# Kernel optimization log

Measured on AMD Instinct MI355X. Metric: run time of the kernel, lower is better.

The kernel has to match this reference:

```python
import jax, jax.numpy as jnp
import numpy as np

B, H, S, D = 1, 16, 4096, 64


def setup_inputs() -> dict:
    key = jax.random.key(0)
    kq, kk, kv = jax.random.split(key, 3)
    Q = jax.random.normal(kq, (B, H, S, D), dtype=jnp.float32)
    K = jax.random.normal(kk, (B, H, S, D), dtype=jnp.float32)
    V = jax.random.normal(kv, (B, H, S, D), dtype=jnp.float32)
    # causal mask, broadcast over batch/heads: True = attend
    mask = jnp.tril(jnp.ones((S, S), dtype=bool))[None, None, :, :]
    return {"Q": Q, "K": K, "V": V, "mask": mask}


def reference(Q, K, V, mask):
    d_k = Q.shape[-1]
    scale = 1.0 / jnp.sqrt(jnp.asarray(d_k, dtype=Q.dtype))
    # [..., q, k] scores; mask==False positions set to -inf before softmax
    scores = jnp.einsum('...qd,...kd->...qk', Q, K) * scale
    scores = jnp.where(mask, scores, jnp.asarray(-jnp.inf, dtype=scores.dtype))
    attn = jax.nn.softmax(scores, axis=-1)
    return jnp.einsum('...qk,...kd->...qd', attn, V)
```

## Files before the change

kernel.cpp:

```cpp
#include <hip/hip_runtime.h>
#include <hip/hip_bf16.h>

typedef __attribute__((ext_vector_type(8))) short short8;
typedef __attribute__((ext_vector_type(4))) short s4v;
typedef __attribute__((ext_vector_type(4))) int   int4v;
typedef __attribute__((ext_vector_type(4))) float floatx4;

#define MFMA16(A,B,C) __builtin_amdgcn_mfma_f32_16x16x32_bf16(A,B,C,0,0,0)

__device__ __forceinline__ short bf16bits(float x) {
    __hip_bfloat16 h = __float2bfloat16(x);
    return *(short*)&h;
}
__device__ __forceinline__ short8 cvt8(const float* p) {
    floatx4 a = *(const floatx4*)p;
    floatx4 b = *(const floatx4*)(p + 4);
    short8 r;
    r[0]=bf16bits(a.x); r[1]=bf16bits(a.y); r[2]=bf16bits(a.z); r[3]=bf16bits(a.w);
    r[4]=bf16bits(b.x); r[5]=bf16bits(b.y); r[6]=bf16bits(b.z); r[7]=bf16bits(b.w);
    return r;
}
__device__ __forceinline__ short8 cvt8s(const float* p) {
    constexpr float SCL2 = 0.125f * 1.44269504088896f;
    floatx4 a = *(const floatx4*)p;
    floatx4 b = *(const floatx4*)(p + 4);
    a *= SCL2; b *= SCL2;
    short8 r;
    r[0]=bf16bits(a.x); r[1]=bf16bits(a.y); r[2]=bf16bits(a.z); r[3]=bf16bits(a.w);
    r[4]=bf16bits(b.x); r[5]=bf16bits(b.y); r[6]=bf16bits(b.z); r[7]=bf16bits(b.w);
    return r;
}
__device__ __forceinline__ int pk2(float lo, float hi) {
    int r;
    asm("v_cvt_pk_bf16_f32 %0, %1, %2" : "=v"(r) : "v"(lo), "v"(hi));
    return r;
}

__global__ __launch_bounds__(256) void prep(const float* __restrict__ V,
                                            short* __restrict__ VT,
                                            const float* __restrict__ K,
                                            short* __restrict__ K16, int doK)
{
    __shared__ short tile[64 * 65];
    const int t  = threadIdx.x;
    const int h  = blockIdx.x >> 6;
    const int s0 = (blockIdx.x & 63) << 6;
    const float* src = V + ((size_t)h * 4096 + s0) * 64;
    const int r = t >> 4, dq = (t & 15) * 4;
#pragma unroll
    for (int pass = 0; pass < 4; ++pass) {
        const int s = pass * 16 + r;
        floatx4 f = *(const floatx4*)(src + s * 64 + dq);
        short* w = tile + s * 65 + dq;
        w[0] = bf16bits(f.x); w[1] = bf16bits(f.y);
        w[2] = bf16bits(f.z); w[3] = bf16bits(f.w);
    }
    __syncthreads();
    const int d = t >> 2, sc = (t & 3) * 16;
    short8 a, b;
#pragma unroll
    for (int j = 0; j < 8; ++j) a[j] = tile[(sc + j) * 65 + d];
#pragma unroll
    for (int j = 0; j < 8; ++j) b[j] = tile[(sc + 8 + j) * 65 + d];
    short* dst = VT + ((size_t)h * 64 + d) * 4096 + s0 + sc;
    *(short8*)dst       = a;
    *(short8*)(dst + 8) = b;
    if (doK) {
        const size_t base = (size_t)blockIdx.x * 4096 + (size_t)t * 16;
        *(short8*)(K16 + base)     = cvt8(K + base);
        *(short8*)(K16 + base + 8) = cvt8(K + base + 8);
    }
}

template<bool KB16>
__global__ __attribute__((amdgpu_waves_per_eu(4, 4))) __launch_bounds__(256)
void attn_fast(const float* __restrict__ Qg, const float* __restrict__ Kg,
               const short* __restrict__ K16g, const short* __restrict__ VTg,
               float* __restrict__ Og)
{
    constexpr int S = 4096, D = 64;

    __shared__ __align__(16) short lK[4096];
    __shared__ __align__(16) short lV[4096];
    __shared__ __align__(16) float lM[5120];

    const int tid = threadIdx.x;
    const int wv  = tid >> 6;
    const int ln  = tid & 63;
    const int ll  = ln & 15;
    const int qd  = ln >> 4;
    const int qhalf = wv & 1;
    const int khalf = wv >> 1;

    const int c = blockIdx.x & 255;
    const int s = blockIdx.x >> 8;
    const int h = c & 15;
    const int x = c >> 4;
    const int qblk = (s == 0) ? (63 - x) : (s == 1) ? (32 + x) : (s == 2) ? (31 - x) : x;
    const int qb   = qblk << 6;
    const int qrow = qb + (qhalf << 5);

    const float* Qh  = Qg  + (size_t)h * S * D;
    const float* Kf  = Kg  + (size_t)h * S * D;
    const short* K16 = K16g + (size_t)h * S * D;
    const short* Vt  = VTg + (size_t)h * 64 * S;

    short8 qA0, qA1, qB0, qB1;
    {
        const float* qp = Qh + (qrow + ll) * D + qd * 8;
        qA0 = cvt8s(qp);       qA1 = cvt8s(qp + 32);
        const float* qp2 = qp + 16 * D;
        qB0 = cvt8s(qp2);      qB1 = cvt8s(qp2 + 32);
    }

    floatx4 oA[4], oB[4], olA, olB;
#pragma unroll
    for (int dt = 0; dt < 4; ++dt) { oA[dt] = (floatx4){0.f,0.f,0.f,0.f}; oB[dt] = oA[dt]; }
    olA = (floatx4){0.f,0.f,0.f,0.f};
    olB = olA;

    short8 ones;
#pragma unroll
    for (int j = 0; j < 8; ++j) ones[j] = (short)0x3F80;

    const int kkey = tid >> 3, kd8 = tid & 7;
    const int koct = kd8 & 3;
    short* kdst = lK + ((kkey >> 4) * 2 + (kd8 >> 2)) * 512
                     + ((((kkey & 15) | (koct << 4)) ^ (koct * 5)) * 8);
    const float* ksrcf = Kf  + kkey * 64 + kd8 * 8;
    const short* ksrc6 = K16 + kkey * 64 + kd8 * 8;
    const int vd = tid >> 2, voct = tid & 3;
    short* vdst = lV + (vd >> 4) * 512
                     + ((((vd & 15) | (voct << 4)) ^ (voct * 5)) * 8);
    const short* vsrc = Vt + (size_t)vd * S + voct * 8;
    const int rblk = ((ll | (qd << 4)) ^ (qd * 5));

    const int kv_end = qb + 64;
    const int wv_end = qrow + 32;

    auto ldK = [&](int kv) -> short8 {
        return KB16 ? *(const short8*)(ksrc6 + kv * 64) : cvt8(ksrcf + kv * 64);
    };

    auto mkpf = [&](floatx4 sc0, floatx4 sc1, int qgrp, int kvh) -> short8 {
        float p0[4], p1[4];
#pragma unroll
        for (int r = 0; r < 4; ++r) { p0[r] = exp2f(sc0[r]); p1[r] = exp2f(sc1[r]); }
        if (kvh + 31 > qgrp) {
            const int qg = qgrp + ll;
            const int k0 = kvh + qd * 4, k1 = k0 + 16;
#pragma unroll
            for (int r = 0; r < 4; ++r) {
                if (k0 + r > qg) p0[r] = 0.f;
                if (k1 + r > qg) p1[r] = 0.f;
            }
        }
        int w0 = pk2(p0[0], p0[1]);
        int w1 = pk2(p0[2], p0[3]);
        int w2 = pk2(p1[0], p1[1]);
        int w3 = pk2(p1[2], p1[3]);
        asm("v_permlane32_swap_b32 %0, %1" : "+v"(w0), "+v"(w2));
        asm("v_permlane32_swap_b32 %0, %1" : "+v"(w1), "+v"(w3));
        asm("v_permlane16_swap_b32 %0, %1" : "+v"(w0), "+v"(w2));
        asm("v_permlane16_swap_b32 %0, %1" : "+v"(w1), "+v"(w3));
        int4v pv = {w0, w1, w2, w3};
        return *(short8*)&pv;
    };

    short8 kpre0 = ldK(0),  kpre1 = ldK(32);
    short8 vpre0 = *(const short8*)(vsrc);
    short8 vpre1 = *(const short8*)(vsrc + 32);

    for (int kv = 0; kv < kv_end; kv += 64) {
        __syncthreads();
        *(short8*)kdst          = kpre0;
        *(short8*)(kdst + 2048) = kpre1;
        *(short8*)vdst          = vpre0;
        *(short8*)(vdst + 2048) = vpre1;
        __syncthreads();
        if (kv + 64 < kv_end) {
            kpre0 = ldK(kv + 64);
            kpre1 = ldK(kv + 96);
            vpre0 = *(const short8*)(vsrc + kv + 64);
            vpre1 = *(const short8*)(vsrc + kv + 96);
        }

        const int kvw = kv + (khalf << 5);
        if (kvw < wv_end) {
            const short* Kb = lK + (khalf << 11);
            const short* Vb = lV + (khalf << 11);
            floatx4 zz = (floatx4){0.f,0.f,0.f,0.f};
            floatx4 sA0=zz, sA1=zz, sB0=zz, sB1=zz;
            short8 kf;
            __builtin_amdgcn_s_setprio(1);
            kf = ((const short8*)(Kb +    0))[rblk]; sA0 = MFMA16(kf, qA0, sA0); sB0 = MFMA16(kf, qB0, sB0);
            kf = ((const short8*)(Kb +  512))[rblk]; sA0 = MFMA16(kf, qA1, sA0); sB0 = MFMA16(kf, qB1, sB0);
            kf = ((const short8*)(Kb + 1024))[rblk]; sA1 = MFMA16(kf, qA0, sA1); sB1 = MFMA16(kf, qB0, sB1);
            kf = ((const short8*)(Kb + 1536))[rblk]; sA1 = MFMA16(kf, qA1, sA1); sB1 = MFMA16(kf, qB1, sB1);
            __builtin_amdgcn_s_setprio(0);

            short8 pfA = mkpf(sA0, sA1, qrow,      kvw);
            short8 pfB = mkpf(sB0, sB1, qrow + 16, kvw);
            __builtin_amdgcn_s_setprio(1);
#pragma unroll
            for (int dt = 0; dt < 4; ++dt) {
                short8 vf = ((const short8*)(Vb + dt * 512))[rblk];
                oA[dt] = MFMA16(pfA, vf, oA[dt]);
                oB[dt] = MFMA16(pfB, vf, oB[dt]);
            }
            olA = MFMA16(pfA, ones, olA);
            olB = MFMA16(pfB, ones, olB);
            __builtin_amdgcn_s_setprio(0);
        }
    }

    __syncthreads();
    const int mbase = ((qhalf << 6) + ln) * 40;
    if (khalf == 1) {
#pragma unroll
        for (int dt = 0; dt < 4; ++dt)
#pragma unroll
            for (int r = 0; r < 4; ++r) {
                lM[mbase + dt * 4 + r]      = oA[dt][r];
                lM[mbase + 20 + dt * 4 + r] = oB[dt][r];
            }
#pragma unroll
        for (int r = 0; r < 4; ++r) {
            lM[mbase + 16 + r] = olA[r];
            lM[mbase + 36 + r] = olB[r];
        }
    }
    __syncthreads();
    if (khalf == 0) {
#pragma unroll
        for (int dt = 0; dt < 4; ++dt)
#pragma unroll
            for (int r = 0; r < 4; ++r) {
                oA[dt][r] += lM[mbase + dt * 4 + r];
                oB[dt][r] += lM[mbase + 20 + dt * 4 + r];
            }
#pragma unroll
        for (int r = 0; r < 4; ++r) {
            olA[r] += lM[mbase + 16 + r];
            olB[r] += lM[mbase + 36 + r];
        }
#pragma unroll
        for (int r = 0; r < 4; ++r) {
            const float rl = 1.f / fmaxf(olA[r], 1e-37f);
            const int q = qrow + qd * 4 + r;
            float* op = Og + ((size_t)h * S + q) * D + ll;
#pragma unroll
            for (int dt = 0; dt < 4; ++dt)
                op[dt * 16] = oA[dt][r] * rl;
        }
#pragma unroll
        for (int r = 0; r < 4; ++r) {
            const float rl = 1.f / fmaxf(olB[r], 1e-37f);
            const int q = qrow + 16 + qd * 4 + r;
            float* op = Og + ((size_t)h * S + q) * D + ll;
#pragma unroll
            for (int dt = 0; dt < 4; ++dt)
                op[dt * 16] = oB[dt][r] * rl;
        }
    }
}

__global__ __launch_bounds__(256, 4)
void attn_legacy(const float* __restrict__ Qg, const float* __restrict__ Kg,
                 const float* __restrict__ Vg, float* __restrict__ Og)
{
    constexpr int S = 4096, D = 64;
    constexpr float SCL2 = 0.125f * 1.44269504088896f;
    constexpr float NEG  = -1.0e30f;
    __shared__ __align__(16) short lK[2048];
    __shared__ __align__(16) short lV[2048];
    __shared__ __align__(16) short lP[2048];
    const int tid = threadIdx.x, wv = tid >> 6, ln = tid & 63, ll = ln & 15, qd = ln >> 4;
    const int bid = blockIdx.x, h = bid & 15, qblk = 63 - (bid >> 4), qb = qblk << 6;
    const float* Qh = Qg + (size_t)h * S * D;
    const float* Kh = Kg + (size_t)h * S * D;
    const float* Vh = Vg + (size_t)h * S * D;
    const int qrow = qb + wv * 16;
    short8 qf0, qf1;
    { const float* qp = Qh + (qrow + ll) * D + qd * 8; qf0 = cvt8(qp); qf1 = cvt8(qp + 32); }
    floatx4 o[4]; float mi[4], li[4];
#pragma unroll
    for (int dt = 0; dt < 4; ++dt) o[dt] = (floatx4){0.f,0.f,0.f,0.f};
#pragma unroll
    for (int r = 0; r < 4; ++r) { mi[r] = NEG; li[r] = 0.f; }
    const int k_st = tid >> 3, dbase = (tid & 7) * 8;
    const int sq = (dbase >> 3) & 3, sks = dbase >> 5;
    const int kw_slot = (((k_st >> 4) * 2 + sks) * 64)
                      + (((sq << 4) | (k_st & 15)) ^ (sq | (sks << 2)));
    const int kr0 = ln ^ qd, kr1 = ln ^ (qd | 4), vbit3 = (ln >> 3) & 1;
    const int kv_end = qb + 64, wv_end = qrow + 16;
    for (int kv = 0; kv < kv_end; kv += 32) {
        __syncthreads();
        {
            short8 kval = cvt8(Kh + (kv + k_st) * D + dbase);
            ((short8*)lK)[kw_slot] = kval;
            short8 vval = cvt8(Vh + (kv + k_st) * D + dbase);
            const int vq = (k_st >> 3) << 4, vj = k_st & 7;
#pragma unroll
            for (int i = 0; i < 8; ++i) {
                int d = dbase + i, dt = d >> 4, l2 = d & 15;
                int lp = (vq | l2) ^ (((l2 >> 3) & 1) | (dt << 1));
                lV[dt * 512 + lp * 8 + vj] = vval[i];
            }
        }
        __syncthreads();
        if (kv < wv_end) {
            floatx4 sc0 = (floatx4){0.f,0.f,0.f,0.f}, sc1 = sc0; short8 kf;
            kf = ((const short8*)lK)[0*64+kr0]; sc0 = MFMA16(qf0, kf, sc0);
            kf = ((const short8*)lK)[1*64+kr1]; sc0 = MFMA16(qf1, kf, sc0);
            kf = ((const short8*)lK)[2*64+kr0]; sc1 = MFMA16(qf0, kf, sc1);
            kf = ((const short8*)lK)[3*64+kr1]; sc1 = MFMA16(qf1, kf, sc1);
            float p0[4], p1[4]; const int qg = qrow + qd * 4;
#pragma unroll
            for (int r = 0; r < 4; ++r) { p0[r] = sc0[r]*SCL2; p1[r] = sc1[r]*SCL2; }
            if (kv + 31 > qrow) {
                const int k0 = kv + ll, k1 = kv + 16 + ll;
#pragma unroll
                for (int r = 0; r < 4; ++r) {
                    if (k0 > qg + r) p0[r] = NEG;
                    if (k1 > qg + r) p1[r] = NEG;
                }
            }
#pragma unroll
            for (int r = 0; r < 4; ++r) {
                float mx = fmaxf(p0[r], p1[r]);
                mx = fmaxf(mx, __shfl_xor(mx,1)); mx = fmaxf(mx, __shfl_xor(mx,2));
                mx = fmaxf(mx, __shfl_xor(mx,4)); mx = fmaxf(mx, __shfl_xor(mx,8));
                const float nm = fmaxf(mi[r], mx);
                const float a = exp2f(mi[r] - nm); mi[r] = nm;
                p0[r] = exp2f(p0[r] - nm); p1[r] = exp2f(p1[r] - nm);
                float ps = p0[r] + p1[r];
                ps += __shfl_xor(ps,1); ps += __shfl_xor(ps,2);
                ps += __shfl_xor(ps,4); ps += __shfl_xor(ps,8);
                li[r] = li[r] * a + ps;
#pragma unroll
                for (int dt = 0; dt < 4; ++dt) o[dt][r] *= a;
            }
            {
                const int pbase = wv * 512 + (ll & 7);
                const int dl0 = ((ll >> 3) << 4) + qd * 4;
#pragma unroll
                for (int r = 0; r < 4; ++r) {
                    lP[pbase + (dl0 + r) * 8]      = bf16bits(p0[r]);
                    lP[pbase + (dl0 + 32 + r) * 8] = bf16bits(p1[r]);
                }
            }
            __threadfence_block();
            short8 pf = ((const short8*)lP)[wv * 64 + ln];
#pragma unroll
            for (int dt = 0; dt < 4; ++dt) {
                short8 vf = ((const short8*)lV)[dt * 64 + (ln ^ (vbit3 | (dt << 1)))];
                o[dt] = MFMA16(pf, vf, o[dt]);
            }
        }
    }
#pragma unroll
    for (int r = 0; r < 4; ++r) {
        const float rl = 1.f / fmaxf(li[r], 1e-30f);
        const int q = qrow + qd * 4 + r;
        float* op = Og + ((size_t)h * S + q) * D + ll;
#pragma unroll
        for (int dt = 0; dt < 4; ++dt) op[dt * 16] = o[dt][r] * rl;
    }
}

extern "C" void kernel_launch(void* const* d_in, const int* in_sizes, int n_in,
                              void* d_out, int out_size, void* d_ws, size_t ws_size,
                              hipStream_t stream) {
    const float* Q = (const float*)d_in[0];
    const float* K = (const float*)d_in[1];
    const float* V = (const float*)d_in[2];
    float* O = (float*)d_out;
    const size_t elems  = (size_t)16 * 4096 * 64;
    const size_t oneBuf = elems * sizeof(short);
    if (ws_size >= 2 * oneBuf) {
        short* VT  = (short*)d_ws;
        short* K16 = (short*)d_ws + elems;
        prep<<<dim3(1024), dim3(256), 0, stream>>>(V, VT, K, K16, 1);
        attn_fast<true><<<dim3(1024), dim3(256), 0, stream>>>(Q, K, K16, VT, O);
    } else if (ws_size >= oneBuf) {
        short* VT = (short*)d_ws;
        prep<<<dim3(1024), dim3(256), 0, stream>>>(V, VT, K, VT, 0);
        attn_fast<false><<<dim3(1024), dim3(256), 0, stream>>>(Q, K, nullptr, VT, O);
    } else {
        attn_legacy<<<dim3(1024), dim3(256), 0, stream>>>(Q, K, V, O);
    }
}
```

Measured before the change: 185.2 us.

## Double-buffer K/V tiles in LDS using direct global-to-LDS loads

Replaces register-staged K/V prefetch with global_load_lds direct transfers into a double-buffered LDS ring, which removes one of the two barriers per iteration and the register round-trip. The source addresses are remapped so the direct-load layout keeps the swizzled pattern. The end-of-kernel reduction scratch now reuses the K/V buffers, and waves_per_eu is raised from 4 to 5. The risks are the larger LDS footprint, the tighter register budget, and correctness of the one-barrier scheme, since the next-buffer writes are ordered only by the single barrier at the top of the loop.

```diff
diff --git a/kernel.cpp b/kernel.cpp
--- a/kernel.cpp
+++ b/kernel.cpp
@@ -34,6 +34,11 @@
     int r;
     asm("v_cvt_pk_bf16_f32 %0, %1, %2" : "=v"(r) : "v"(lo), "v"(hi));
     return r;
+}
+__device__ __forceinline__ void g2l16(const short* g, short* l) {
+    __builtin_amdgcn_global_load_lds(
+        (const __attribute__((address_space(1))) void*)g,
+        (__attribute__((address_space(3))) void*)l, 16, 0, 0);
 }
 
 __global__ __launch_bounds__(256) void prep(const float* __restrict__ V,
@@ -73,16 +78,15 @@
 }
 
 template<bool KB16>
-__global__ __attribute__((amdgpu_waves_per_eu(4, 4))) __launch_bounds__(256)
+__global__ __attribute__((amdgpu_waves_per_eu(5, 5))) __launch_bounds__(256)
 void attn_fast(const float* __restrict__ Qg, const float* __restrict__ Kg,
                const short* __restrict__ K16g, const short* __restrict__ VTg,
                float* __restrict__ Og)
 {
     constexpr int S = 4096, D = 64;
 
-    __shared__ __align__(16) short lK[4096];
-    __shared__ __align__(16) short lV[4096];
-    __shared__ __align__(16) float lM[5120];
+    __shared__ __align__(16) short lK[8192];
+    __shared__ __align__(16) short lV[8192];
 
     const int tid = threadIdx.x;
     const int wv  = tid >> 6;
@@ -123,24 +127,29 @@
 #pragma unroll
     for (int j = 0; j < 8; ++j) ones[j] = (short)0x3F80;
 
-    const int kkey = tid >> 3, kd8 = tid & 7;
-    const int koct = kd8 & 3;
-    short* kdst = lK + ((kkey >> 4) * 2 + (kd8 >> 2)) * 512
-                     + ((((kkey & 15) | (koct << 4)) ^ (koct * 5)) * 8);
-    const float* ksrcf = Kf  + kkey * 64 + kd8 * 8;
-    const short* ksrc6 = K16 + kkey * 64 + kd8 * 8;
-    const int vd = tid >> 2, voct = tid & 3;
-    short* vdst = lV + (vd >> 4) * 512
-                     + ((((vd & 15) | (voct << 4)) ^ (voct * 5)) * 8);
-    const short* vsrc = Vt + (size_t)vd * S + voct * 8;
+    int kOff0, kOff1, vOff0, vOff1;
+    const float *kFp0, *kFp1;
+#define DECODE_SLOT(J, KOF, VOF, KFP) {                                        \
+        const int slot = (wv * 2 + (J)) * 64 + ln;                             \
+        const int hh = slot >> 8, bb = (slot >> 6) & 3, sw = slot & 63;        \
+        const int ko = (sw >> 4) & 3;                                          \
+        const int kkey = hh * 32 + (bb >> 1) * 16 + ((sw ^ (ko * 5)) & 15);    \
+        const int kd8  = ((bb & 1) << 2) | ko;                                 \
+        const int vd   = bb * 16 + ((sw ^ (ko * 5)) & 15);                     \
+        KOF = kkey * 64 + kd8 * 8;                                             \
+        VOF = vd * S + hh * 32 + ko * 8;                                       \
+        KFP = Kf + (size_t)kkey * D + kd8 * 8;                                 \
+    }
+    DECODE_SLOT(0, kOff0, vOff0, kFp0)
+    DECODE_SLOT(1, kOff1, vOff1, kFp1)
+#undef DECODE_SLOT
+    const int dstA = (wv * 2 + 0) * 512;
+    const int dstB = (wv * 2 + 1) * 512;
+
     const int rblk = ((ll | (qd << 4)) ^ (qd * 5));
 
     const int kv_end = qb + 64;
     const int wv_end = qrow + 32;
-
-    auto ldK = [&](int kv) -> short8 {
-        return KB16 ? *(const short8*)(ksrc6 + kv * 64) : cvt8(ksrcf + kv * 64);
-    };
 
     auto mkpf = [&](floatx4 sc0, floatx4 sc1, int qgrp, int kvh) -> short8 {
         float p0[4], p1[4];
@@ -167,28 +176,47 @@
         return *(short8*)&pv;
     };
 
-    short8 kpre0 = ldK(0),  kpre1 = ldK(32);
-    short8 vpre0 = *(const short8*)(vsrc);
-    short8 vpre1 = *(const short8*)(vsrc + 32);
-
+    short8 kApre, kBpre;
+    g2l16(Vt + vOff0, lV + dstA);
+    g2l16(Vt + vOff1, lV + dstB);
+    if constexpr (KB16) {
+        g2l16(K16 + kOff0, lK + dstA);
+        g2l16(K16 + kOff1, lK + dstB);
+    } else {
+        *(short8*)(lK + dstA + ln * 8) = cvt8(kFp0);
+        *(short8*)(lK + dstB + ln * 8) = cvt8(kFp1);
+        if (64 < kv_end) {
+            kApre = cvt8(kFp0 + (size_t)64 * D);
+            kBpre = cvt8(kFp1 + (size_t)64 * D);
+        }
+    }
+
+    int bo = 0;
     for (int kv = 0; kv < kv_end; kv += 64) {
         __syncthreads();
-        *(short8*)kdst          = kpre0;
-        *(short8*)(kdst + 2048) = kpre1;
-        *(short8*)vdst          = vpre0;
-        *(short8*)(vdst + 2048) = vpre1;
-        __syncthreads();
+        const int nbo = bo ^ 4096;
         if (kv + 64 < kv_end) {
-            kpre0 = ldK(kv + 64);
-            kpre1 = ldK(kv + 96);
-            vpre0 = *(const short8*)(vsrc + kv + 64);
-            vpre1 = *(const short8*)(vsrc + kv + 96);
+            const short* Vs = Vt + (kv + 64);
+            g2l16(Vs + vOff0, lV + nbo + dstA);
+            g2l16(Vs + vOff1, lV + nbo + dstB);
+            if constexpr (KB16) {
+                const short* Ks = K16 + (size_t)(kv + 64) * 64;
+                g2l16(Ks + kOff0, lK + nbo + dstA);
+                g2l16(Ks + kOff1, lK + nbo + dstB);
+            } else {
+                *(short8*)(lK + nbo + dstA + ln * 8) = kApre;
+                *(short8*)(lK + nbo + dstB + ln * 8) = kBpre;
+                if (kv + 128 < kv_end) {
+                    kApre = cvt8(kFp0 + (size_t)(kv + 128) * D);
+                    kBpre = cvt8(kFp1 + (size_t)(kv + 128) * D);
+                }
+            }
         }
 
         const int kvw = kv + (khalf << 5);
         if (kvw < wv_end) {
-            const short* Kb = lK + (khalf << 11);
-            const short* Vb = lV + (khalf << 11);
+            const short* Kb = lK + bo + (khalf << 11);
+            const short* Vb = lV + bo + (khalf << 11);
             floatx4 zz = (floatx4){0.f,0.f,0.f,0.f};
             floatx4 sA0=zz, sA1=zz, sB0=zz, sB1=zz;
             short8 kf;
@@ -212,22 +240,25 @@
             olB = MFMA16(pfB, ones, olB);
             __builtin_amdgcn_s_setprio(0);
         }
+        bo = nbo;
     }
 
     __syncthreads();
-    const int mbase = ((qhalf << 6) + ln) * 40;
+    float* sAod = (float*)lK;
+    float* sBod = (float*)lV;
+    const int mbase = ((qhalf << 6) + ln) * 20;
     if (khalf == 1) {
 #pragma unroll
         for (int dt = 0; dt < 4; ++dt)
 #pragma unroll
             for (int r = 0; r < 4; ++r) {
-                lM[mbase + dt * 4 + r]      = oA[dt][r];
-                lM[mbase + 20 + dt * 4 + r] = oB[dt][r];
+                sAod[mbase + dt * 4 + r] = oA[dt][r];
+                sBod[mbase + dt * 4 + r] = oB[dt][r];
             }
 #pragma unroll
         for (int r = 0; r < 4; ++r) {
-            lM[mbase + 16 + r] = olA[r];
-            lM[mbase + 36 + r] = olB[r];
+            sAod[mbase + 16 + r] = olA[r];
+            sBod[mbase + 16 + r] = olB[r];
         }
     }
     __syncthreads();
@@ -236,13 +267,13 @@
         for (int dt = 0; dt < 4; ++dt)
 #pragma unroll
             for (int r = 0; r < 4; ++r) {
-                oA[dt][r] += lM[mbase + dt * 4 + r];
-                oB[dt][r] += lM[mbase + 20 + dt * 4 + r];
+                oA[dt][r] += sAod[mbase + dt * 4 + r];
+                oB[dt][r] += sBod[mbase + dt * 4 + r];
             }
 #pragma unroll
         for (int r = 0; r < 4; ++r) {
-            olA[r] += lM[mbase + 16 + r];
-            olB[r] += lM[mbase + 36 + r];
+            olA[r] += sAod[mbase + 16 + r];
+            olB[r] += sBod[mbase + 16 + r];
         }
 #pragma unroll
         for (int r = 0; r < 4; ++r) {
```

Result: slower. 266.1 us (+43.7%).

## Double-buffer K/V shared tiles to drop one barrier per iteration

Applied to the files above, without the earlier changes.

Converts the single-buffered LDS K/V staging into a ping-pong double buffer, so each iteration writes the next tile into one half while computing on the previous tile from the other half. This removes the second __syncthreads per tile and lets LDS stores overlap MFMA work. The merge scratch buffer is folded into the now-larger K/V arrays, so total LDS usage stays similar. The cost is one extra loop iteration of pipeline skew and somewhat more complex indexing.

```diff
diff --git a/kernel.cpp b/kernel.cpp
--- a/kernel.cpp
+++ b/kernel.cpp
@@ -80,9 +80,8 @@
 {
     constexpr int S = 4096, D = 64;
 
-    __shared__ __align__(16) short lK[4096];
-    __shared__ __align__(16) short lV[4096];
-    __shared__ __align__(16) float lM[5120];
+    __shared__ __align__(16) short lK[8192];
+    __shared__ __align__(16) short lV[8192];
 
     const int tid = threadIdx.x;
     const int wv  = tid >> 6;
@@ -167,67 +166,77 @@
         return *(short8*)&pv;
     };
 
-    short8 kpre0 = ldK(0),  kpre1 = ldK(32);
-    short8 vpre0 = *(const short8*)(vsrc);
-    short8 vpre1 = *(const short8*)(vsrc + 32);
-
-    for (int kv = 0; kv < kv_end; kv += 64) {
+    short8 kp0 = ldK(0),  kp1 = ldK(32);
+    short8 vp0 = *(const short8*)(vsrc);
+    short8 vp1 = *(const short8*)(vsrc + 32);
+
+    const int ntiles = kv_end >> 6;
+    int bo = 0;
+    for (int t = 0; t <= ntiles; ++t) {
         __syncthreads();
-        *(short8*)kdst          = kpre0;
-        *(short8*)(kdst + 2048) = kpre1;
-        *(short8*)vdst          = vpre0;
-        *(short8*)(vdst + 2048) = vpre1;
-        __syncthreads();
-        if (kv + 64 < kv_end) {
-            kpre0 = ldK(kv + 64);
-            kpre1 = ldK(kv + 96);
-            vpre0 = *(const short8*)(vsrc + kv + 64);
-            vpre1 = *(const short8*)(vsrc + kv + 96);
-        }
-
-        const int kvw = kv + (khalf << 5);
-        if (kvw < wv_end) {
-            const short* Kb = lK + (khalf << 11);
-            const short* Vb = lV + (khalf << 11);
-            floatx4 zz = (floatx4){0.f,0.f,0.f,0.f};
-            floatx4 sA0=zz, sA1=zz, sB0=zz, sB1=zz;
-            short8 kf;
-            __builtin_amdgcn_s_setprio(1);
-            kf = ((const short8*)(Kb +    0))[rblk]; sA0 = MFMA16(kf, qA0, sA0); sB0 = MFMA16(kf, qB0, sB0);
-            kf = ((const short8*)(Kb +  512))[rblk]; sA0 = MFMA16(kf, qA1, sA0); sB0 = MFMA16(kf, qB1, sB0);
-            kf = ((const short8*)(Kb + 1024))[rblk]; sA1 = MFMA16(kf, qA0, sA1); sB1 = MFMA16(kf, qB0, sB1);
-            kf = ((const short8*)(Kb + 1536))[rblk]; sA1 = MFMA16(kf, qA1, sA1); sB1 = MFMA16(kf, qB1, sB1);
-            __builtin_amdgcn_s_setprio(0);
-
-            short8 pfA = mkpf(sA0, sA1, qrow,      kvw);
-            short8 pfB = mkpf(sB0, sB1, qrow + 16, kvw);
-            __builtin_amdgcn_s_setprio(1);
-#pragma unroll
-            for (int dt = 0; dt < 4; ++dt) {
-                short8 vf = ((const short8*)(Vb + dt * 512))[rblk];
-                oA[dt] = MFMA16(pfA, vf, oA[dt]);
-                oB[dt] = MFMA16(pfB, vf, oB[dt]);
-            }
-            olA = MFMA16(pfA, ones, olA);
-            olB = MFMA16(pfB, ones, olB);
-            __builtin_amdgcn_s_setprio(0);
-        }
+        if (t < ntiles) {
+            *(short8*)(kdst + bo)        = kp0;
+            *(short8*)(kdst + bo + 2048) = kp1;
+            *(short8*)(vdst + bo)        = vp0;
+            *(short8*)(vdst + bo + 2048) = vp1;
+            const int nk = (t + 1) << 6;
+            if (nk < kv_end) {
+                kp0 = ldK(nk);
+                kp1 = ldK(nk + 32);
+                vp0 = *(const short8*)(vsrc + nk);
+                vp1 = *(const short8*)(vsrc + nk + 32);
+            }
+        }
+        if (t > 0) {
+            const int kv  = (t - 1) << 6;
+            const int kvw = kv + (khalf << 5);
+            if (kvw < wv_end) {
+                const int ro = (bo ^ 4096) + (khalf << 11);
+                const short* Kb = lK + ro;
+                const short* Vb = lV + ro;
+                floatx4 zz = (floatx4){0.f,0.f,0.f,0.f};
+                floatx4 sA0=zz, sA1=zz, sB0=zz, sB1=zz;
+                short8 kf;
+                __builtin_amdgcn_s_setprio(1);
+                kf = ((const short8*)(Kb +    0))[rblk]; sA0 = MFMA16(kf, qA0, sA0); sB0 = MFMA16(kf, qB0, sB0);
+                kf = ((const short8*)(Kb +  512))[rblk]; sA0 = MFMA16(kf, qA1, sA0); sB0 = MFMA16(kf, qB1, sB0);
+                kf = ((const short8*)(Kb + 1024))[rblk]; sA1 = MFMA16(kf, qA0, sA1); sB1 = MFMA16(kf, qB0, sB1);
+                kf = ((const short8*)(Kb + 1536))[rblk]; sA1 = MFMA16(kf, qA1, sA1); sB1 = MFMA16(kf, qB1, sB1);
+                __builtin_amdgcn_s_setprio(0);
+
+                short8 pfA = mkpf(sA0, sA1, qrow,      kvw);
+                short8 pfB = mkpf(sB0, sB1, qrow + 16, kvw);
+                __builtin_amdgcn_s_setprio(1);
+#pragma unroll
+                for (int dt = 0; dt < 4; ++dt) {
+                    short8 vf = ((const short8*)(Vb + dt * 512))[rblk];
+                    oA[dt] = MFMA16(pfA, vf, oA[dt]);
+                    oB[dt] = MFMA16(pfB, vf, oB[dt]);
+                }
+                olA = MFMA16(pfA, ones, olA);
+                olB = MFMA16(pfB, ones, olB);
+                __builtin_amdgcn_s_setprio(0);
+            }
+        }
+        bo ^= 4096;
     }
 
     __syncthreads();
-    const int mbase = ((qhalf << 6) + ln) * 40;
+    float* sAod = (float*)lK;
+    float* sBod = (float*)lV;
+    const int mbase = ((qhalf << 6) + ln) * 20;
     if (khalf == 1) {
 #pragma unroll
         for (int dt = 0; dt < 4; ++dt)
 #pragma unroll
             for (int r = 0; r < 4; ++r) {
-                lM[mbase + dt * 4 + r]      = oA[dt][r];
-                lM[mbase + 20 + dt * 4 + r] = oB[dt][r];
+                sAod[mbase + dt * 4 + r] = oA[dt][r];
+                sBod[mbase + dt * 4 + r] = oB[dt][r];
             }
 #pragma unroll
         for (int r = 0; r < 4; ++r) {
-            lM[mbase + 16 + r] = olA[r];
-            lM[mbase + 36 + r] = olB[r];
+            sAod[mbase + 16 + r] = olA[r];
+            sBod[mbase + 16 + r] = olB[r];
         }
     }
     __syncthreads();
@@ -236,13 +245,13 @@
         for (int dt = 0; dt < 4; ++dt)
 #pragma unroll
             for (int r = 0; r < 4; ++r) {
-                oA[dt][r] += lM[mbase + dt * 4 + r];
-                oB[dt][r] += lM[mbase + 20 + dt * 4 + r];
+                oA[dt][r] += sAod[mbase + dt * 4 + r];
+                oB[dt][r] += sBod[mbase + dt * 4 + r];
             }
 #pragma unroll
         for (int r = 0; r < 4; ++r) {
-            olA[r] += lM[mbase + 16 + r];
-            olB[r] += lM[mbase + 36 + r];
+            olA[r] += sAod[mbase + 16 + r];
+            olB[r] += sBod[mbase + 16 + r];
         }
 #pragma unroll
         for (int r = 0; r < 4; ++r) {
```

Result: no change. 184.4 us (-0.4%).
